# Kernel optimization log

Hardware: AMD Instinct MI355X
Metric: run time of the kernel (lower is better)

Reference implementation:

```python
import jax, jax.numpy as jnp
import numpy as np

HIDDEN = 2048
HEADS = 16
LN_EPS = 1e-5


def setup_inputs() -> dict:
    key = jax.random.key(0)
    ks = jax.random.split(key, 12)
    B, S, D = 4, 4096, HIDDEN
    std = 0.02
    inp = {
        "x": jax.random.normal(ks[0], (B, S, D), dtype=jnp.float32),
        "ln_g": jnp.ones((D,), dtype=jnp.float32),
        "ln_b": jnp.zeros((D,), dtype=jnp.float32),
        # weights stored as [in, out] so y = x @ W + b (equivalent to torch Linear)
        "Wq": jax.random.normal(ks[1], (D, D), dtype=jnp.float32) * std,
        "bq": jnp.zeros((D,), dtype=jnp.float32),
        "Wk": jax.random.normal(ks[2], (D, D), dtype=jnp.float32) * std,
        "bk": jnp.zeros((D,), dtype=jnp.float32),
        "Wv": jax.random.normal(ks[3], (D, D), dtype=jnp.float32) * std,
        "bv": jnp.zeros((D,), dtype=jnp.float32),
        "Wo": jax.random.normal(ks[4], (D, D), dtype=jnp.float32) * std,
        "bo": jnp.zeros((D,), dtype=jnp.float32),
    }
    return inp


def reference(x, ln_g, ln_b, Wq, bq, Wk, bk, Wv, bv, Wo, bo):
    B, S, D = x.shape
    H = HEADS
    hd = D // H
    # LayerNorm
    mu = jnp.mean(x, axis=-1, keepdims=True)
    var = jnp.mean(jnp.square(x - mu), axis=-1, keepdims=True)
    xn = (x - mu) * jax.lax.rsqrt(var + LN_EPS) * ln_g + ln_b
    # QKV projections
    q = (xn @ Wq + bq).reshape(B, S, H, hd)
    k = (xn @ Wk + bk).reshape(B, S, H, hd)
    v = (xn @ Wv + bv).reshape(B, S, H, hd)
    # Faithful to source: q @ k.transpose(-2,-1) on [B,S,H,hd] -> scores [B,S,H,H]
    # (attention mixes across heads per token; scale uses full hidden_dim)
    scores = jnp.einsum('bshd,bsgd->bshg', q, k) / jnp.sqrt(jnp.float32(D))
    weights = jax.nn.softmax(scores, axis=-1)
    context = jnp.einsum('bshg,bsgd->bshd', weights, v).reshape(B, S, D)
    out = context @ Wo + bo
    return out
```

## Files before the change

kernel.cpp:

```cpp
#include <hip/hip_runtime.h>

typedef __bf16 bf16x8 __attribute__((ext_vector_type(8)));
typedef __bf16 bf16x4 __attribute__((ext_vector_type(4)));
typedef float  f32x4  __attribute__((ext_vector_type(4)));

#define GLOAD_LDS16(g, l) \
  __builtin_amdgcn_global_load_lds((const __attribute__((address_space(1))) void*)(g), \
                                   (__attribute__((address_space(3))) void*)(l), 16, 0, 0)

__global__ __launch_bounds__(256) void wcvt_kernel(
    const float* __restrict__ W0, const float* __restrict__ W1,
    const float* __restrict__ W2, const float* __restrict__ W3,
    __bf16* __restrict__ WtBase)
{
  const float* W = (blockIdx.z == 0) ? W0 : (blockIdx.z == 1) ? W1 : (blockIdx.z == 2) ? W2 : W3;
  __bf16* dst = WtBase + (size_t)blockIdx.z * 2048 * 2048;
  __shared__ float tile[32][33];
  const int tx = threadIdx.x & 31, ty = threadIdx.x >> 5;
  const int gi = blockIdx.x * 32, gj = blockIdx.y * 32;
  #pragma unroll
  for (int r = 0; r < 32; r += 8)
    tile[ty + r][tx] = W[(size_t)(gi + ty + r) * 2048 + gj + tx];
  __syncthreads();
  #pragma unroll
  for (int r = 0; r < 32; r += 8)
    dst[(size_t)(gj + ty + r) * 2048 + gi + tx] = (__bf16)tile[tx][ty + r];
}

__global__ __launch_bounds__(256) void ln_kernel(
    const float* __restrict__ x, const float* __restrict__ gw,
    const float* __restrict__ bw, __bf16* __restrict__ xn)
{
  __shared__ float red[8];
  const size_t base = (size_t)blockIdx.x * 2048;
  const int t = threadIdx.x;
  float4 v0 = *(const float4*)(x + base + t * 4);
  float4 v1 = *(const float4*)(x + base + 1024 + t * 4);
  float sm = v0.x + v0.y + v0.z + v0.w + v1.x + v1.y + v1.z + v1.w;
  float sq = v0.x*v0.x + v0.y*v0.y + v0.z*v0.z + v0.w*v0.w
           + v1.x*v1.x + v1.y*v1.y + v1.z*v1.z + v1.w*v1.w;
  #pragma unroll
  for (int off = 32; off; off >>= 1) {
    sm += __shfl_down(sm, off);
    sq += __shfl_down(sq, off);
  }
  if ((t & 63) == 0) { red[t >> 6] = sm; red[4 + (t >> 6)] = sq; }
  __syncthreads();
  const float fs = red[0] + red[1] + red[2] + red[3];
  const float fq = red[4] + red[5] + red[6] + red[7];
  const float mu = fs * (1.f / 2048.f);
  const float var = fq * (1.f / 2048.f) - mu * mu;
  const float rs = rsqrtf(var + 1e-5f);
  float4 g0 = *(const float4*)(gw + t * 4);
  float4 g1 = *(const float4*)(gw + 1024 + t * 4);
  float4 b0 = *(const float4*)(bw + t * 4);
  float4 b1 = *(const float4*)(bw + 1024 + t * 4);
  bf16x4 o0, o1;
  o0[0] = (__bf16)((v0.x - mu) * rs * g0.x + b0.x);
  o0[1] = (__bf16)((v0.y - mu) * rs * g0.y + b0.y);
  o0[2] = (__bf16)((v0.z - mu) * rs * g0.z + b0.z);
  o0[3] = (__bf16)((v0.w - mu) * rs * g0.w + b0.w);
  o1[0] = (__bf16)((v1.x - mu) * rs * g1.x + b1.x);
  o1[1] = (__bf16)((v1.y - mu) * rs * g1.y + b1.y);
  o1[2] = (__bf16)((v1.z - mu) * rs * g1.z + b1.z);
  o1[3] = (__bf16)((v1.w - mu) * rs * g1.w + b1.w);
  *(bf16x4*)(xn + base + t * 4) = o0;
  *(bf16x4*)(xn + base + 1024 + t * 4) = o1;
}

template <int MODE>
__global__ __launch_bounds__(512, 2) void gemm256(
    const __bf16* __restrict__ A, int lda,
    const __bf16* __restrict__ WtBase,
    const float* __restrict__ b0, const float* __restrict__ b1,
    const float* __restrict__ b2, void* __restrict__ outp)
{
  __shared__ __attribute__((aligned(16))) char smem[131072];
  const int tid = threadIdx.x, lane = tid & 63, wid = tid >> 6;
  const int wm = wid >> 2, wn = wid & 3;
  const int m0 = blockIdx.x * 256;
  int which, n0;
  const __bf16* Bt;
  const float* bias;
  if (MODE == 0) {
    which = blockIdx.y >> 3;
    n0 = (blockIdx.y & 7) * 256;
    Bt = WtBase + (size_t)which * 2048 * 2048 + (size_t)n0 * 2048;
    bias = (which == 0) ? b0 : (which == 1) ? b1 : b2;
  } else {
    which = 0;
    n0 = blockIdx.y * 256;
    Bt = WtBase + (size_t)n0 * 2048;
    bias = b0;
  }

  const int lr0 = tid >> 3;
  const int sg  = (tid & 7) ^ (lr0 & 7);
  const __bf16* Ag0 = A + (size_t)(m0 + lr0) * lda + sg * 8;
  const __bf16* Ag1 = A + (size_t)(m0 + 64 + lr0) * lda + sg * 8;
  const __bf16* Bg0 = Bt + (size_t)((lr0 >> 5) * 64 + (lr0 & 31)) * 2048 + sg * 8;
  const __bf16* Bg1 = Bt + (size_t)((lr0 >> 5) * 64 + 32 + (lr0 & 31)) * 2048 + sg * 8;
  const int ldst = __builtin_amdgcn_readfirstlane(wid * 1024);

#define STAGE_A(H, DBB, KT)                                                        \
  do {                                                                             \
    GLOAD_LDS16(Ag##H + (KT) * 64, smem + (DBB) + (H) * 16384 + ldst);             \
    GLOAD_LDS16(Ag##H + (size_t)128 * lda + (KT) * 64,                             \
                smem + (DBB) + (H) * 16384 + 8192 + ldst);                         \
  } while (0)
#define STAGE_B(H, DBB, KT)                                                        \
  do {                                                                             \
    GLOAD_LDS16(Bg##H + (KT) * 64, smem + (DBB) + 32768 + (H) * 16384 + ldst);     \
    GLOAD_LDS16(Bg##H + 262144 + (KT) * 64,                                        \
                smem + (DBB) + 32768 + (H) * 16384 + 8192 + ldst);                 \
  } while (0)

  const int fr = lane & 15, sl = lane >> 4, x7 = fr & 7;
  const int aoff0 = (wm * 64 + fr) * 128 + ((sl) ^ x7) * 16;
  const int aoff1 = (wm * 64 + fr) * 128 + ((4 + sl) ^ x7) * 16;
  const int boff0 = (wn * 32 + fr) * 128 + ((sl) ^ x7) * 16;
  const int boff1 = (wn * 32 + fr) * 128 + ((4 + sl) ^ x7) * 16;

  bf16x8 afr[4][2], bfr0[2][2], bfr1[2][2];
  f32x4 acc[8][4];
  #pragma unroll
  for (int i = 0; i < 8; i++)
    #pragma unroll
    for (int j = 0; j < 4; j++) acc[i][j] = (f32x4){0.f, 0.f, 0.f, 0.f};

#define READ_A(MH, DB)                                                             \
  _Pragma("unroll") for (int mi = 0; mi < 4; mi++)                                 \
  _Pragma("unroll") for (int kk = 0; kk < 2; kk++)                                 \
    afr[mi][kk] = *(const bf16x8*)(smem + (DB) + (MH) * 16384 +                    \
                                   (kk ? aoff1 : aoff0) + mi * 2048);
#define READ_B(NH, DB, DEST)                                                       \
  _Pragma("unroll") for (int ni = 0; ni < 2; ni++)                                 \
  _Pragma("unroll") for (int kk = 0; kk < 2; kk++)                                 \
    DEST[ni][kk] = *(const bf16x8*)(smem + (DB) + 32768 + (NH) * 16384 +           \
                                    (kk ? boff1 : boff0) + ni * 2048);
#define MFMA16(MH, NH, BSET)                                                       \
  _Pragma("unroll") for (int kk = 0; kk < 2; kk++)                                 \
  _Pragma("unroll") for (int mi = 0; mi < 4; mi++)                                 \
  _Pragma("unroll") for (int ni = 0; ni < 2; ni++)                                 \
    acc[(MH) * 4 + mi][(NH) * 2 + ni] = __builtin_amdgcn_mfma_f32_16x16x32_bf16(   \
        afr[mi][kk], BSET[ni][kk], acc[(MH) * 4 + mi][(NH) * 2 + ni], 0, 0, 0);
#define PHASE_TAIL(MH, NH, BSET)                                                   \
  __builtin_amdgcn_s_barrier();                                                    \
  asm volatile("s_waitcnt lgkmcnt(0)" ::: "memory");                               \
  __builtin_amdgcn_s_setprio(1);                                                   \
  MFMA16(MH, NH, BSET);                                                            \
  __builtin_amdgcn_s_setprio(0);                                                   \
  __builtin_amdgcn_s_barrier();

  STAGE_A(0, 0, 0);
  STAGE_B(0, 0, 0);
  STAGE_A(1, 0, 0);
  STAGE_B(1, 0, 0);
  STAGE_A(0, 65536, 1);
  STAGE_B(0, 65536, 1);
  STAGE_B(1, 65536, 1);
  __syncthreads();

  const int NT = 32;
  for (int kt = 0; kt < NT; kt++) {
    const int db  = (kt & 1) << 16;
    const int dbn = db ^ 65536;
    if (kt == NT - 1) { asm volatile("s_waitcnt vmcnt(0)" ::: "memory"); }
    else              { asm volatile("s_waitcnt vmcnt(6)" ::: "memory"); }
    READ_A(0, db);
    READ_B(0, db, bfr0);
    if (kt + 1 < NT) STAGE_A(1, dbn, kt + 1);
    PHASE_TAIL(0, 0, bfr0);
    READ_B(1, db, bfr1);
    if (kt + 2 < NT) STAGE_A(0, db, kt + 2);
    PHASE_TAIL(0, 1, bfr1);
    READ_A(1, db);
    if (kt + 2 < NT) STAGE_B(0, db, kt + 2);
    PHASE_TAIL(1, 1, bfr1);
    if (kt + 2 < NT) STAGE_B(1, db, kt + 2);
    PHASE_TAIL(1, 0, bfr0);
  }
#undef STAGE_A
#undef STAGE_B
#undef READ_A
#undef READ_B
#undef MFMA16
#undef PHASE_TAIL

  const int colf = lane & 15, rowf = (lane >> 4) * 4;
  #pragma unroll
  for (int mi = 0; mi < 8; mi++) {
    const int rw = m0 + wm * 128 + mi * 16 + rowf;
    #pragma unroll
    for (int ni = 0; ni < 4; ni++) {
      const int cc = n0 + wn * 64 + ni * 16 + colf;
      const float bi = bias[cc];
      if (MODE == 0) {
        __bf16* qkv = (__bf16*)outp;
        #pragma unroll
        for (int j = 0; j < 4; j++)
          qkv[(size_t)(rw + j) * 6144 + (size_t)which * 2048 + cc] =
              (__bf16)(acc[mi][ni][j] + bi);
      } else {
        float* out = (float*)outp;
        #pragma unroll
        for (int j = 0; j < 4; j++)
          out[(size_t)(rw + j) * 2048 + cc] = acc[mi][ni][j] + bi;
      }
    }
  }
}

__global__ __launch_bounds__(256) void attn_kernel(__bf16* __restrict__ qkv)
{
  __shared__ __bf16 att[4 * 6144];
  __shared__ float Psh[4 * 256];
  const int tid = threadIdx.x, lane = tid & 63, w = tid >> 6;
  const size_t token = (size_t)blockIdx.x * 4 + w;
  const __bf16* src = qkv + token * 6144;
  char* ldsb = (char*)att;
  const int lbase = __builtin_amdgcn_readfirstlane(w * 12288);
  #pragma unroll
  for (int r = 0; r < 12; r++)
    GLOAD_LDS16(src + r * 512 + lane * 8, ldsb + lbase + r * 1024);
  __syncthreads();

  const __bf16* my = att + w * 6144;
  const int h = lane >> 2, gq = lane & 3;
  const __bf16* qrow = my + h * 128;
  float s[4] = {0.f, 0.f, 0.f, 0.f};
  for (int d = 0; d < 128; d += 8) {
    bf16x8 qv = *(const bf16x8*)(qrow + d);
    float qf[8];
    #pragma unroll
    for (int j = 0; j < 8; j++) qf[j] = (float)qv[j];
    #pragma unroll
    for (int i = 0; i < 4; i++) {
      bf16x8 kv = *(const bf16x8*)(my + 2048 + (gq * 4 + i) * 128 + d);
      #pragma unroll
      for (int j = 0; j < 8; j++) s[i] += qf[j] * (float)kv[j];
    }
  }
  const float scale = 0.022097086912079612f;
  #pragma unroll
  for (int i = 0; i < 4; i++) s[i] *= scale;
  float mx = fmaxf(fmaxf(s[0], s[1]), fmaxf(s[2], s[3]));
  mx = fmaxf(mx, __shfl_xor(mx, 1));
  mx = fmaxf(mx, __shfl_xor(mx, 2));
  float p[4], sum = 0.f;
  #pragma unroll
  for (int i = 0; i < 4; i++) { p[i] = __expf(s[i] - mx); sum += p[i]; }
  sum += __shfl_xor(sum, 1);
  sum += __shfl_xor(sum, 2);
  const float inv = 1.f / sum;
  #pragma unroll
  for (int i = 0; i < 4; i++) Psh[w * 256 + h * 16 + gq * 4 + i] = p[i] * inv;
  __syncthreads();

  const int h2 = lane >> 2, db = (lane & 3) * 32;
  const __bf16* vb = my + 4096;
  float acc[32];
  #pragma unroll
  for (int i = 0; i < 32; i++) acc[i] = 0.f;
  for (int g = 0; g < 16; g++) {
    const float pv = Psh[w * 256 + h2 * 16 + g];
    #pragma unroll
    for (int c = 0; c < 4; c++) {
      bf16x8 vv = *(const bf16x8*)(vb + g * 128 + db + c * 8);
      #pragma unroll
      for (int j = 0; j < 8; j++) acc[c * 8 + j] += pv * (float)vv[j];
    }
  }
  __bf16* dst = qkv + token * 6144 + h2 * 128 + db;
  #pragma unroll
  for (int c = 0; c < 4; c++) {
    bf16x8 ov;
    #pragma unroll
    for (int j = 0; j < 8; j++) ov[j] = (__bf16)acc[c * 8 + j];
    *(bf16x8*)(dst + c * 8) = ov;
  }
}

extern "C" void kernel_launch(void* const* d_in, const int* in_sizes, int n_in,
                              void* d_out, int out_size, void* d_ws, size_t ws_size,
                              hipStream_t stream)
{
  const float* x    = (const float*)d_in[0];
  const float* ln_g = (const float*)d_in[1];
  const float* ln_b = (const float*)d_in[2];
  const float* Wq   = (const float*)d_in[3];
  const float* bq   = (const float*)d_in[4];
  const float* Wk   = (const float*)d_in[5];
  const float* bk   = (const float*)d_in[6];
  const float* Wv   = (const float*)d_in[7];
  const float* bv   = (const float*)d_in[8];
  const float* Wo   = (const float*)d_in[9];
  const float* bo   = (const float*)d_in[10];
  float* out = (float*)d_out;
  const int M = in_sizes[0] / 2048;

  char* ws = (char*)d_ws;
  __bf16* Wt  = (__bf16*)ws;
  __bf16* qkv = (__bf16*)(ws + 33554432);
  __bf16* xn  = (__bf16*)d_out;

  wcvt_kernel<<<dim3(64, 64, 4), 256, 0, stream>>>(Wq, Wk, Wv, Wo, Wt);
  ln_kernel<<<M, 256, 0, stream>>>(x, ln_g, ln_b, xn);
  gemm256<0><<<dim3(M / 256, 24), 512, 0, stream>>>(xn, 2048, Wt, bq, bk, bv, (void*)qkv);
  attn_kernel<<<M / 4, 256, 0, stream>>>(qkv);
  gemm256<1><<<dim3(M / 256, 8), 512, 0, stream>>>(qkv, 6144, Wt + (size_t)3 * 2048 * 2048,
                                                   bo, nullptr, nullptr, (void*)out);
}
```

Measured before the change: 623.0 us.

## Software-pipeline LDS fragment reads into MFMA phases of bf16 GEMM mainloop

Restructures the GEMM k-loop so LDS fragment reads for the next phase (and the next k-tile's A0/B0 fragments) are issued inside the previous MFMA phase. It uses double register sets for the A and B fragments, unrolls the loop by two to alternate those buffers, relaxes the vmcnt wait, and peels the last two tiles into an epilogue without conditional staging. The aim is to hide LDS latency behind MFMA work and drop per-phase conditionals. In exchange it uses more VGPRs, which may lower occupancy, and depends on subtle barrier/waitcnt correctness.

```diff
diff --git a/kernel.cpp b/kernel.cpp
--- a/kernel.cpp
+++ b/kernel.cpp
@@ -121,36 +121,61 @@
   const int boff0 = (wn * 32 + fr) * 128 + ((sl) ^ x7) * 16;
   const int boff1 = (wn * 32 + fr) * 128 + ((4 + sl) ^ x7) * 16;
 
-  bf16x8 afr[4][2], bfr0[2][2], bfr1[2][2];
+  bf16x8 afrA[4][2], afrB[4][2], bfr1[2][2], bfr0e[2][2], bfr0o[2][2];
   f32x4 acc[8][4];
   #pragma unroll
   for (int i = 0; i < 8; i++)
     #pragma unroll
     for (int j = 0; j < 4; j++) acc[i][j] = (f32x4){0.f, 0.f, 0.f, 0.f};
 
-#define READ_A(MH, DB)                                                             \
+#define READ_A_INTO(DEST, MH, DB)                                                  \
   _Pragma("unroll") for (int mi = 0; mi < 4; mi++)                                 \
   _Pragma("unroll") for (int kk = 0; kk < 2; kk++)                                 \
-    afr[mi][kk] = *(const bf16x8*)(smem + (DB) + (MH) * 16384 +                    \
-                                   (kk ? aoff1 : aoff0) + mi * 2048);
-#define READ_B(NH, DB, DEST)                                                       \
+    DEST[mi][kk] = *(const bf16x8*)(smem + (DB) + (MH) * 16384 +                   \
+                                    (kk ? aoff1 : aoff0) + mi * 2048);
+#define READ_B_INTO(DEST, NH, DB)                                                  \
   _Pragma("unroll") for (int ni = 0; ni < 2; ni++)                                 \
   _Pragma("unroll") for (int kk = 0; kk < 2; kk++)                                 \
     DEST[ni][kk] = *(const bf16x8*)(smem + (DB) + 32768 + (NH) * 16384 +           \
                                     (kk ? boff1 : boff0) + ni * 2048);
-#define MFMA16(MH, NH, BSET)                                                       \
+#define MFMA16(MH, NH, ASET, BSET)                                                 \
   _Pragma("unroll") for (int kk = 0; kk < 2; kk++)                                 \
   _Pragma("unroll") for (int mi = 0; mi < 4; mi++)                                 \
   _Pragma("unroll") for (int ni = 0; ni < 2; ni++)                                 \
     acc[(MH) * 4 + mi][(NH) * 2 + ni] = __builtin_amdgcn_mfma_f32_16x16x32_bf16(   \
-        afr[mi][kk], BSET[ni][kk], acc[(MH) * 4 + mi][(NH) * 2 + ni], 0, 0, 0);
-#define PHASE_TAIL(MH, NH, BSET)                                                   \
-  __builtin_amdgcn_s_barrier();                                                    \
-  asm volatile("s_waitcnt lgkmcnt(0)" ::: "memory");                               \
-  __builtin_amdgcn_s_setprio(1);                                                   \
-  MFMA16(MH, NH, BSET);                                                            \
-  __builtin_amdgcn_s_setprio(0);                                                   \
-  __builtin_amdgcn_s_barrier();
+        ASET[mi][kk], BSET[ni][kk], acc[(MH) * 4 + mi][(NH) * 2 + ni], 0, 0, 0);
+
+#define VM10 asm volatile("s_waitcnt vmcnt(10)" ::: "memory")
+#define LGKM0 asm volatile("s_waitcnt lgkmcnt(0)" ::: "memory")
+#define BAR __builtin_amdgcn_s_barrier()
+#define PRIO1 __builtin_amdgcn_s_setprio(1)
+#define PRIO0 __builtin_amdgcn_s_setprio(0)
+
+#define KTILE(KT, DB, DBN, B0CUR, B0NXT)                                           \
+                                                                           \
+  STAGE_A(1, DBN, (KT) + 1);                                                       \
+  VM10; BAR; LGKM0; PRIO1;                                                         \
+  READ_B_INTO(bfr1, 1, DB);                                                        \
+  MFMA16(0, 0, afrA, B0CUR);                                                       \
+  PRIO0; BAR;                                                                      \
+                                                                           \
+  STAGE_A(0, DB, (KT) + 2);                                                        \
+  VM10; BAR; LGKM0; PRIO1;                                                         \
+  READ_A_INTO(afrB, 1, DB);                                                        \
+  MFMA16(0, 1, afrA, bfr1);                                                        \
+  PRIO0; BAR;                                                                      \
+                                                      \
+  STAGE_B(0, DB, (KT) + 2);                                                        \
+  BAR; LGKM0; PRIO1;                                                               \
+  MFMA16(1, 1, afrB, bfr1);                                                        \
+  PRIO0; BAR;                                                                      \
+                                                                           \
+  STAGE_B(1, DB, (KT) + 2);                                                        \
+  VM10; BAR; LGKM0; PRIO1;                                                         \
+  READ_A_INTO(afrA, 0, DBN);                                                       \
+  READ_B_INTO(B0NXT, 0, DBN);                                                      \
+  MFMA16(1, 0, afrB, B0CUR);                                                       \
+  PRIO0; BAR;
 
   STAGE_A(0, 0, 0);
   STAGE_B(0, 0, 0);
@@ -160,32 +185,43 @@
   STAGE_B(0, 65536, 1);
   STAGE_B(1, 65536, 1);
   __syncthreads();
-
-  const int NT = 32;
-  for (int kt = 0; kt < NT; kt++) {
-    const int db  = (kt & 1) << 16;
-    const int dbn = db ^ 65536;
-    if (kt == NT - 1) { asm volatile("s_waitcnt vmcnt(0)" ::: "memory"); }
-    else              { asm volatile("s_waitcnt vmcnt(6)" ::: "memory"); }
-    READ_A(0, db);
-    READ_B(0, db, bfr0);
-    if (kt + 1 < NT) STAGE_A(1, dbn, kt + 1);
-    PHASE_TAIL(0, 0, bfr0);
-    READ_B(1, db, bfr1);
-    if (kt + 2 < NT) STAGE_A(0, db, kt + 2);
-    PHASE_TAIL(0, 1, bfr1);
-    READ_A(1, db);
-    if (kt + 2 < NT) STAGE_B(0, db, kt + 2);
-    PHASE_TAIL(1, 1, bfr1);
-    if (kt + 2 < NT) STAGE_B(1, db, kt + 2);
-    PHASE_TAIL(1, 0, bfr0);
-  }
+  READ_A_INTO(afrA, 0, 0);
+  READ_B_INTO(bfr0e, 0, 0);
+
+  for (int kt = 0; kt < 30; kt += 2) {
+    KTILE(kt, 0, 65536, bfr0e, bfr0o);
+    KTILE((kt + 1), 65536, 0, bfr0o, bfr0e);
+  }
+
+  STAGE_A(1, 65536, 31);
+  asm volatile("s_waitcnt vmcnt(0)" ::: "memory");
+  __syncthreads();
+#define TAILTILE(DB)                                                               \
+  READ_A_INTO(afrA, 0, DB);                                                        \
+  READ_B_INTO(bfr0e, 0, DB);                                                       \
+  LGKM0;                                                                           \
+  MFMA16(0, 0, afrA, bfr0e);                                                       \
+  READ_B_INTO(bfr1, 1, DB);                                                        \
+  LGKM0;                                                                           \
+  MFMA16(0, 1, afrA, bfr1);                                                        \
+  READ_A_INTO(afrB, 1, DB);                                                        \
+  LGKM0;                                                                           \
+  MFMA16(1, 1, afrB, bfr1);                                                        \
+  MFMA16(1, 0, afrB, bfr0e);
+  TAILTILE(0);
+  TAILTILE(65536);
+#undef TAILTILE
+#undef KTILE
 #undef STAGE_A
 #undef STAGE_B
-#undef READ_A
-#undef READ_B
+#undef READ_A_INTO
+#undef READ_B_INTO
 #undef MFMA16
-#undef PHASE_TAIL
+#undef VM10
+#undef LGKM0
+#undef BAR
+#undef PRIO1
+#undef PRIO0
 
   const int colf = lane & 15, rowf = (lane >> 4) * 4;
   #pragma unroll
```

After: 610.3 us. 1.02x faster.
